# Performance work log

Hardware: AMD Instinct MI355X
Metric: run time of the kernel (lower is better)

## Reference

```python
import jax, jax.numpy as jnp
import numpy as np

B, L, H_IN, H_RED, H_MLP = 2, 1024, 768, 128, 256

def setup_inputs() -> dict:
    key = jax.random.key(0)
    ks = jax.random.split(key, 7)
    s_in = 1.0 / np.sqrt(H_IN)
    s_p = 1.0 / np.sqrt(2 * H_RED)
    s_m = 1.0 / np.sqrt(H_MLP)
    return {
        "inputs": jax.random.normal(ks[0], (B, L, H_IN), dtype=jnp.float32),
        "Wr": jax.random.uniform(ks[1], (H_RED, H_IN), jnp.float32, -s_in, s_in),
        "br": jax.random.uniform(ks[2], (H_RED,), jnp.float32, -s_in, s_in),
        "W1": jax.random.uniform(ks[3], (H_MLP, 2 * H_RED), jnp.float32, -s_p, s_p),
        "b1": jax.random.uniform(ks[4], (H_MLP,), jnp.float32, -s_p, s_p),
        "W2": jax.random.uniform(ks[5], (1, H_MLP), jnp.float32, -s_m, s_m),
        "b2": jax.random.uniform(ks[6], (1,), jnp.float32, -s_m, s_m),
    }

def reference(inputs, Wr, br, W1, b1, W2, b2):
    # pre_reduction: [B,L,H_IN] -> [B,L,H_RED]
    e = jnp.einsum("blh,rh->blr", inputs, Wr) + br
    b_, l_, r_ = e.shape
    # pairwise concat: row i gets e[i], col j gets e[j] -> [B,L,L,2R]
    row = jnp.broadcast_to(e[:, :, None, :], (b_, l_, l_, r_))
    col = jnp.broadcast_to(e[:, None, :, :], (b_, l_, l_, r_))
    pair = jnp.concatenate([row, col], axis=-1)
    # Lin2D: Linear(2R,256) -> ReLU -> Linear(256,1)
    h = jax.nn.relu(jnp.einsum("bijc,mc->bijm", pair, W1) + b1)
    out = jnp.einsum("bijm,om->bijo", h, W2) + b2  # [B,L,L,1]
    out = out[..., 0]  # [B,L,L]
    # symmetrize: triu(out) + triu(out,1)^T
    upper = jnp.triu(out)
    lower = jnp.swapaxes(jnp.triu(out, k=1), -1, -2)
    return upper + lower
```

## Files before the change

kernel.cpp:

```cpp
#include <hip/hip_runtime.h>

typedef __attribute__((ext_vector_type(4))) float f32x4;
typedef __attribute__((ext_vector_type(8))) short bf16x8;

__device__ inline unsigned short f2bf(float x) {
  unsigned u = __builtin_bit_cast(unsigned, x);
  u += 0x7fffu + ((u >> 16) & 1u);
  return (unsigned short)(u >> 16);
}

__device__ inline bf16x8 cvt8(const float* __restrict__ p) {
  f32x4 lo = *(const f32x4*)p;
  f32x4 hi = *(const f32x4*)(p + 4);
  bf16x8 r;
  r[0] = (short)f2bf(lo[0]); r[1] = (short)f2bf(lo[1]);
  r[2] = (short)f2bf(lo[2]); r[3] = (short)f2bf(lo[3]);
  r[4] = (short)f2bf(hi[0]); r[5] = (short)f2bf(hi[1]);
  r[6] = (short)f2bf(hi[2]); r[7] = (short)f2bf(hi[3]);
  return r;
}

__global__ __launch_bounds__(256) void gemm1_kernel(
    const float* __restrict__ X, const float* __restrict__ Wr,
    const float* __restrict__ br, unsigned short* __restrict__ Ebf) {
  int wave = threadIdx.x >> 6;
  int lane = threadIdx.x & 63;
  int t0 = (blockIdx.x * 4 + wave) * 16;
  int n0 = blockIdx.y * 16;
  int lrow = lane & 15;
  int kgrp = (lane >> 4) * 8;
  const float* arow = X + (size_t)(t0 + lrow) * 768 + kgrp;
  const float* brow = Wr + (size_t)(n0 + lrow) * 768 + kgrp;
  f32x4 acc = {0.f, 0.f, 0.f, 0.f};
  for (int k0 = 0; k0 < 768; k0 += 32) {
    bf16x8 a = cvt8(arow + k0);
    bf16x8 b = cvt8(brow + k0);
    acc = __builtin_amdgcn_mfma_f32_16x16x32_bf16(a, b, acc, 0, 0, 0);
  }
  int cn = lane & 15;
  int rbase = (lane >> 4) * 4;
  float bias = br[n0 + cn];
#pragma unroll
  for (int r = 0; r < 4; ++r) {
    float val = acc[r] + bias;
    Ebf[(size_t)(t0 + rbase + r) * 128 + n0 + cn] = f2bf(val);
  }
}

__global__ __launch_bounds__(256) void gemm2_kernel(
    const unsigned short* __restrict__ Ebf, const float* __restrict__ W1,
    const float* __restrict__ b1, float* __restrict__ UVt) {
  int wave = threadIdx.x >> 6;
  int lane = threadIdx.x & 63;
  int t0 = blockIdx.x * 64 + wave * 16;
  int m0 = blockIdx.y * 16;
  int lidx = lane & 15;
  int kg = (lane >> 4) * 8;
  const float* aBase = (m0 < 256)
      ? (W1 + (size_t)(m0 + lidx) * 256 + kg)
      : (W1 + (size_t)(m0 - 256 + lidx) * 256 + 128 + kg);
  const unsigned short* bBase = Ebf + (size_t)(t0 + lidx) * 128 + kg;
  f32x4 acc = {0.f, 0.f, 0.f, 0.f};
  for (int k0 = 0; k0 < 128; k0 += 32) {
    bf16x8 a = cvt8(aBase + k0);
    bf16x8 b = *(const bf16x8*)(const void*)(bBase + k0);
    acc = __builtin_amdgcn_mfma_f32_16x16x32_bf16(a, b, acc, 0, 0, 0);
  }
  int ct = lane & 15;
  int rb = (lane >> 4) * 4;
#pragma unroll
  for (int r = 0; r < 4; ++r) {
    int m = m0 + rb + r;
    float bias = (m < 256) ? b1[m] : 0.f;
    UVt[(size_t)m * 2048 + t0 + ct] = acc[r] + bias;
  }
}

__global__ __launch_bounds__(256) void pairwise_kernel(
    const float* __restrict__ UVt, const float* __restrict__ W2,
    const float* __restrict__ b2p, float* __restrict__ Out) {
  __shared__ float u_lds[64][32];
  __shared__ float v_lds[64][32];
  __shared__ float w2_lds[256];
  __shared__ float t_lds[32][36];

  int tid = threadIdx.x;
  int b = blockIdx.y;
  int p = blockIdx.x;
  int it = 0;
  while (p >= 32 - it) { p -= 32 - it; ++it; }
  int jt = it + p;

  w2_lds[tid] = W2[tid];

  int tx = tid & 15, ty = tid >> 4;
  int q = tid & 7, row = tid >> 3;
  int utok = b * 1024 + it * 32;
  int vtok = b * 1024 + jt * 32;

  float acc00 = 0.f, acc01 = 0.f, acc10 = 0.f, acc11 = 0.f;

  for (int mc = 0; mc < 4; ++mc) {
    __syncthreads();
#pragma unroll
    for (int ph = 0; ph < 2; ++ph) {
      int ml = row + 32 * ph;
      int mg = mc * 64 + ml;
      f32x4 uu = *(const f32x4*)(UVt + (size_t)mg * 2048 + utok + 4 * q);
      f32x4 vv = *(const f32x4*)(UVt + (size_t)(256 + mg) * 2048 + vtok + 4 * q);
      *(f32x4*)&u_lds[ml][4 * q] = uu;
      *(f32x4*)&v_lds[ml][4 * q] = vv;
    }
    __syncthreads();
    for (int mm = 0; mm < 64; mm += 4) {
      f32x4 w2v = *(const f32x4*)&w2_lds[mc * 64 + mm];
#pragma unroll
      for (int t = 0; t < 4; ++t) {
        float u0 = u_lds[mm + t][2 * ty];
        float u1 = u_lds[mm + t][2 * ty + 1];
        float v0 = v_lds[mm + t][2 * tx];
        float v1 = v_lds[mm + t][2 * tx + 1];
        float w = w2v[t];
        acc00 = fmaf(fmaxf(u0 + v0, 0.f), w, acc00);
        acc01 = fmaf(fmaxf(u0 + v1, 0.f), w, acc01);
        acc10 = fmaf(fmaxf(u1 + v0, 0.f), w, acc10);
        acc11 = fmaf(fmaxf(u1 + v1, 0.f), w, acc11);
      }
    }
  }

  float b2v = b2p[0];
  __syncthreads();
  t_lds[2 * ty][2 * tx] = acc00 + b2v;
  t_lds[2 * ty][2 * tx + 1] = acc01 + b2v;
  t_lds[2 * ty + 1][2 * tx] = acc10 + b2v;
  t_lds[2 * ty + 1][2 * tx + 1] = acc11 + b2v;
  __syncthreads();

  int il = tid >> 3;
  int jq = tid & 7;
  size_t obase = (size_t)b << 20;
  if (it != jt) {
    f32x4 dv, mv;
#pragma unroll
    for (int k = 0; k < 4; ++k) dv[k] = t_lds[il][4 * jq + k];
    *(f32x4*)(Out + obase + (size_t)(it * 32 + il) * 1024 + jt * 32 + 4 * jq) = dv;
#pragma unroll
    for (int k = 0; k < 4; ++k) mv[k] = t_lds[4 * jq + k][il];
    *(f32x4*)(Out + obase + (size_t)(jt * 32 + il) * 1024 + it * 32 + 4 * jq) = mv;
  } else {
#pragma unroll
    for (int k = 0; k < 4; ++k) {
      int jl = 4 * jq + k;
      float v = t_lds[il][jl];
      if (jl >= il) Out[obase + (size_t)(it * 32 + il) * 1024 + jt * 32 + jl] = v;
      if (jl > il)  Out[obase + (size_t)(jt * 32 + jl) * 1024 + it * 32 + il] = v;
    }
  }
}

extern "C" void kernel_launch(void* const* d_in, const int* in_sizes, int n_in,
                              void* d_out, int out_size, void* d_ws, size_t ws_size,
                              hipStream_t stream) {
  (void)in_sizes; (void)n_in; (void)out_size; (void)ws_size;
  const float* X  = (const float*)d_in[0];
  const float* Wr = (const float*)d_in[1];
  const float* br = (const float*)d_in[2];
  const float* W1 = (const float*)d_in[3];
  const float* b1 = (const float*)d_in[4];
  const float* W2 = (const float*)d_in[5];
  const float* b2 = (const float*)d_in[6];
  float* Out = (float*)d_out;

  unsigned short* Ebf = (unsigned short*)d_ws;
  float* UVt = (float*)((char*)d_ws + (size_t)2048 * 128 * 2);

  gemm1_kernel<<<dim3(32, 8), 256, 0, stream>>>(X, Wr, br, Ebf);
  gemm2_kernel<<<dim3(32, 32), 256, 0, stream>>>(Ebf, W1, b1, UVt);
  pairwise_kernel<<<dim3(528, 2), 256, 0, stream>>>(UVt, W2, b2, Out);
}
```

Baseline: 57.71 us.

## Use relu=(x+|x|)/2 split, LDS-tiled GEMMs, and smaller pairwise tiles

The pairwise ReLU is rewritten as 0.5*(x+|x|). The linear part is precomputed per token in a new cvec kernel, leaving only one fabs-add-fma per element in the O(L^2) loop. gemm1 now stages bf16 tiles in LDS with register prefetch and computes 64x64 tiles per block, and gemm2 reuses each W1 fragment across four token tiles. The pairwise kernel moves to 16x16 tiles with 64-thread blocks and vectorized LDS reads, which adds an extra launch and changes occupancy and tile overheads.

```diff
diff --git a/kernel.cpp b/kernel.cpp
--- a/kernel.cpp
+++ b/kernel.cpp
@@ -9,9 +9,7 @@
   return (unsigned short)(u >> 16);
 }
 
-__device__ inline bf16x8 cvt8(const float* __restrict__ p) {
-  f32x4 lo = *(const f32x4*)p;
-  f32x4 hi = *(const f32x4*)(p + 4);
+__device__ inline bf16x8 pack8(f32x4 lo, f32x4 hi) {
   bf16x8 r;
   r[0] = (short)f2bf(lo[0]); r[1] = (short)f2bf(lo[1]);
   r[2] = (short)f2bf(lo[2]); r[3] = (short)f2bf(lo[3]);
@@ -20,141 +18,211 @@
   return r;
 }
 
+__device__ inline bf16x8 cvt8(const float* __restrict__ p) {
+  return pack8(*(const f32x4*)p, *(const f32x4*)(p + 4));
+}
+
 __global__ __launch_bounds__(256) void gemm1_kernel(
     const float* __restrict__ X, const float* __restrict__ Wr,
     const float* __restrict__ br, unsigned short* __restrict__ Ebf) {
-  int wave = threadIdx.x >> 6;
-  int lane = threadIdx.x & 63;
-  int t0 = (blockIdx.x * 4 + wave) * 16;
-  int n0 = blockIdx.y * 16;
-  int lrow = lane & 15;
-  int kgrp = (lane >> 4) * 8;
-  const float* arow = X + (size_t)(t0 + lrow) * 768 + kgrp;
-  const float* brow = Wr + (size_t)(n0 + lrow) * 768 + kgrp;
-  f32x4 acc = {0.f, 0.f, 0.f, 0.f};
-  for (int k0 = 0; k0 < 768; k0 += 32) {
-    bf16x8 a = cvt8(arow + k0);
-    bf16x8 b = cvt8(brow + k0);
-    acc = __builtin_amdgcn_mfma_f32_16x16x32_bf16(a, b, acc, 0, 0, 0);
-  }
-  int cn = lane & 15;
-  int rbase = (lane >> 4) * 4;
-  float bias = br[n0 + cn];
-#pragma unroll
-  for (int r = 0; r < 4; ++r) {
-    float val = acc[r] + bias;
-    Ebf[(size_t)(t0 + rbase + r) * 128 + n0 + cn] = f2bf(val);
+  __shared__ unsigned short Xs[64][40];
+  __shared__ unsigned short Ws[64][40];
+
+  int tid = threadIdx.x;
+  int wave = tid >> 6, lane = tid & 63;
+  int tok0 = blockIdx.x * 64;
+  int n0 = blockIdx.y * 64;
+
+  int srow = tid >> 2;
+  int scol = (tid & 3) * 8;
+  const float* xp = X + (size_t)(tok0 + srow) * 768 + scol;
+  const float* wp = Wr + (size_t)(n0 + srow) * 768 + scol;
+
+  int lr = lane & 15;
+  int kg = (lane >> 4) * 8;
+
+  f32x4 acc0 = {0,0,0,0}, acc1 = {0,0,0,0}, acc2 = {0,0,0,0}, acc3 = {0,0,0,0};
+
+  f32x4 x0 = *(const f32x4*)xp;
+  f32x4 x1 = *(const f32x4*)(xp + 4);
+  f32x4 w0 = *(const f32x4*)wp;
+  f32x4 w1 = *(const f32x4*)(wp + 4);
+
+  for (int ks = 0; ks < 24; ++ks) {
+    __syncthreads();
+    *(bf16x8*)&Xs[srow][scol] = pack8(x0, x1);
+    *(bf16x8*)&Ws[srow][scol] = pack8(w0, w1);
+    __syncthreads();
+    if (ks < 23) {
+      int off = (ks + 1) * 32;
+      x0 = *(const f32x4*)(xp + off);
+      x1 = *(const f32x4*)(xp + off + 4);
+      w0 = *(const f32x4*)(wp + off);
+      w1 = *(const f32x4*)(wp + off + 4);
+    }
+    bf16x8 a = *(const bf16x8*)&Xs[wave * 16 + lr][kg];
+    bf16x8 b0 = *(const bf16x8*)&Ws[lr][kg];
+    bf16x8 b1 = *(const bf16x8*)&Ws[16 + lr][kg];
+    bf16x8 b2v = *(const bf16x8*)&Ws[32 + lr][kg];
+    bf16x8 b3 = *(const bf16x8*)&Ws[48 + lr][kg];
+    acc0 = __builtin_amdgcn_mfma_f32_16x16x32_bf16(a, b0, acc0, 0, 0, 0);
+    acc1 = __builtin_amdgcn_mfma_f32_16x16x32_bf16(a, b1, acc1, 0, 0, 0);
+    acc2 = __builtin_amdgcn_mfma_f32_16x16x32_bf16(a, b2v, acc2, 0, 0, 0);
+    acc3 = __builtin_amdgcn_mfma_f32_16x16x32_bf16(a, b3, acc3, 0, 0, 0);
+  }
+
+  int rb = (lane >> 4) * 4;
+  f32x4 accs[4] = {acc0, acc1, acc2, acc3};
+#pragma unroll
+  for (int t = 0; t < 4; ++t) {
+    int n = n0 + t * 16 + lr;
+    float bias = br[n];
+#pragma unroll
+    for (int r = 0; r < 4; ++r) {
+      int tok = tok0 + wave * 16 + rb + r;
+      Ebf[(size_t)tok * 128 + n] = f2bf(accs[t][r] + bias);
+    }
   }
 }
 
 __global__ __launch_bounds__(256) void gemm2_kernel(
     const unsigned short* __restrict__ Ebf, const float* __restrict__ W1,
     const float* __restrict__ b1, float* __restrict__ UVt) {
-  int wave = threadIdx.x >> 6;
-  int lane = threadIdx.x & 63;
-  int t0 = blockIdx.x * 64 + wave * 16;
-  int m0 = blockIdx.y * 16;
-  int lidx = lane & 15;
-  int kg = (lane >> 4) * 8;
+  int wave = threadIdx.x >> 6, lane = threadIdx.x & 63;
+  int t0 = blockIdx.x * 64;
+  int m0 = (blockIdx.y * 4 + wave) * 16;
+  int lr = lane & 15, kg = (lane >> 4) * 8;
   const float* aBase = (m0 < 256)
-      ? (W1 + (size_t)(m0 + lidx) * 256 + kg)
-      : (W1 + (size_t)(m0 - 256 + lidx) * 256 + 128 + kg);
-  const unsigned short* bBase = Ebf + (size_t)(t0 + lidx) * 128 + kg;
-  f32x4 acc = {0.f, 0.f, 0.f, 0.f};
+      ? (W1 + (size_t)(m0 + lr) * 256 + kg)
+      : (W1 + (size_t)(m0 - 256 + lr) * 256 + 128 + kg);
+  f32x4 acc[4] = {{0,0,0,0},{0,0,0,0},{0,0,0,0},{0,0,0,0}};
+#pragma unroll
   for (int k0 = 0; k0 < 128; k0 += 32) {
     bf16x8 a = cvt8(aBase + k0);
-    bf16x8 b = *(const bf16x8*)(const void*)(bBase + k0);
-    acc = __builtin_amdgcn_mfma_f32_16x16x32_bf16(a, b, acc, 0, 0, 0);
-  }
-  int ct = lane & 15;
+#pragma unroll
+    for (int t = 0; t < 4; ++t) {
+      bf16x8 b = *(const bf16x8*)(const void*)(Ebf + (size_t)(t0 + t * 16 + lr) * 128 + kg + k0);
+      acc[t] = __builtin_amdgcn_mfma_f32_16x16x32_bf16(a, b, acc[t], 0, 0, 0);
+    }
+  }
   int rb = (lane >> 4) * 4;
 #pragma unroll
-  for (int r = 0; r < 4; ++r) {
-    int m = m0 + rb + r;
-    float bias = (m < 256) ? b1[m] : 0.f;
-    UVt[(size_t)m * 2048 + t0 + ct] = acc[r] + bias;
-  }
-}
-
-__global__ __launch_bounds__(256) void pairwise_kernel(
+  for (int t = 0; t < 4; ++t) {
+#pragma unroll
+    for (int r = 0; r < 4; ++r) {
+      int m = m0 + rb + r;
+      float bias = (m < 256) ? b1[m] : 0.f;
+      UVt[(size_t)m * 2048 + t0 + t * 16 + lr] = acc[t][r] + bias;
+    }
+  }
+}
+
+__global__ __launch_bounds__(256) void cvec_kernel(
     const float* __restrict__ UVt, const float* __restrict__ W2,
-    const float* __restrict__ b2p, float* __restrict__ Out) {
-  __shared__ float u_lds[64][32];
-  __shared__ float v_lds[64][32];
-  __shared__ float w2_lds[256];
-  __shared__ float t_lds[32][36];
+    const float* __restrict__ b2p, float* __restrict__ cvec) {
+  int h = blockIdx.y;
+  int tok = blockIdx.x * 256 + threadIdx.x;
+  const float* base = UVt + (size_t)h * 256 * 2048 + tok;
+  float a0 = 0.f, a1 = 0.f, a2 = 0.f, a3 = 0.f;
+#pragma unroll 4
+  for (int m = 0; m < 256; m += 4) {
+    a0 = fmaf(W2[m], base[(size_t)m * 2048], a0);
+    a1 = fmaf(W2[m + 1], base[(size_t)(m + 1) * 2048], a1);
+    a2 = fmaf(W2[m + 2], base[(size_t)(m + 2) * 2048], a2);
+    a3 = fmaf(W2[m + 3], base[(size_t)(m + 3) * 2048], a3);
+  }
+  float r = 0.5f * ((a0 + a1) + (a2 + a3)) + (h == 0 ? b2p[0] : 0.f);
+  cvec[h * 2048 + tok] = r;
+}
+
+__global__ __launch_bounds__(64) void pairwise_kernel(
+    const float* __restrict__ UVt, const float* __restrict__ W2,
+    const float* __restrict__ cvec, float* __restrict__ Out) {
+  __shared__ float u_s[16][132];
+  __shared__ float v_s[16][132];
+  __shared__ float w2_s[256];
+  __shared__ float t_s[16][17];
 
   int tid = threadIdx.x;
   int b = blockIdx.y;
   int p = blockIdx.x;
   int it = 0;
-  while (p >= 32 - it) { p -= 32 - it; ++it; }
+  while (p >= 64 - it) { p -= 64 - it; ++it; }
   int jt = it + p;
 
-  w2_lds[tid] = W2[tid];
-
-  int tx = tid & 15, ty = tid >> 4;
-  int q = tid & 7, row = tid >> 3;
-  int utok = b * 1024 + it * 32;
-  int vtok = b * 1024 + jt * 32;
+  *(f32x4*)&w2_s[4 * tid] = *(const f32x4*)&W2[4 * tid];
+
+  int tx = tid & 7, ty = tid >> 3;
+  int utok = b * 1024 + it * 16;
+  int vtok = b * 1024 + jt * 16;
+
+  int mrow = tid >> 2;
+  int tokq = (tid & 3) * 4;
 
   float acc00 = 0.f, acc01 = 0.f, acc10 = 0.f, acc11 = 0.f;
 
-  for (int mc = 0; mc < 4; ++mc) {
-    __syncthreads();
-#pragma unroll
-    for (int ph = 0; ph < 2; ++ph) {
-      int ml = row + 32 * ph;
-      int mg = mc * 64 + ml;
-      f32x4 uu = *(const f32x4*)(UVt + (size_t)mg * 2048 + utok + 4 * q);
-      f32x4 vv = *(const f32x4*)(UVt + (size_t)(256 + mg) * 2048 + vtok + 4 * q);
-      *(f32x4*)&u_lds[ml][4 * q] = uu;
-      *(f32x4*)&v_lds[ml][4 * q] = vv;
-    }
-    __syncthreads();
-    for (int mm = 0; mm < 64; mm += 4) {
-      f32x4 w2v = *(const f32x4*)&w2_lds[mc * 64 + mm];
-#pragma unroll
-      for (int t = 0; t < 4; ++t) {
-        float u0 = u_lds[mm + t][2 * ty];
-        float u1 = u_lds[mm + t][2 * ty + 1];
-        float v0 = v_lds[mm + t][2 * tx];
-        float v1 = v_lds[mm + t][2 * tx + 1];
-        float w = w2v[t];
-        acc00 = fmaf(fmaxf(u0 + v0, 0.f), w, acc00);
-        acc01 = fmaf(fmaxf(u0 + v1, 0.f), w, acc01);
-        acc10 = fmaf(fmaxf(u1 + v0, 0.f), w, acc10);
-        acc11 = fmaf(fmaxf(u1 + v1, 0.f), w, acc11);
+  for (int mc = 0; mc < 2; ++mc) {
+    int M0 = mc * 128;
+    __syncthreads();
+#pragma unroll
+    for (int g = 0; g < 8; ++g) {
+      int ml = g * 16 + mrow;
+      int m = M0 + ml;
+      f32x4 uu = *(const f32x4*)(UVt + (size_t)m * 2048 + utok + tokq);
+      f32x4 vv = *(const f32x4*)(UVt + (size_t)(256 + m) * 2048 + vtok + tokq);
+#pragma unroll
+      for (int k = 0; k < 4; ++k) {
+        u_s[tokq + k][ml] = uu[k];
+        v_s[tokq + k][ml] = vv[k];
       }
     }
-  }
-
-  float b2v = b2p[0];
+    __syncthreads();
+#pragma unroll 8
+    for (int g = 0; g < 32; ++g) {
+      f32x4 wv = *(const f32x4*)&w2_s[M0 + 4 * g];
+      f32x4 ua = *(const f32x4*)&u_s[2 * ty][4 * g];
+      f32x4 ub = *(const f32x4*)&u_s[2 * ty + 1][4 * g];
+      f32x4 va = *(const f32x4*)&v_s[2 * tx][4 * g];
+      f32x4 vb = *(const f32x4*)&v_s[2 * tx + 1][4 * g];
+#pragma unroll
+      for (int k = 0; k < 4; ++k) {
+        acc00 = fmaf(wv[k], fabsf(ua[k] + va[k]), acc00);
+        acc01 = fmaf(wv[k], fabsf(ua[k] + vb[k]), acc01);
+        acc10 = fmaf(wv[k], fabsf(ub[k] + va[k]), acc10);
+        acc11 = fmaf(wv[k], fabsf(ub[k] + vb[k]), acc11);
+      }
+    }
+  }
+
+  float cu0 = cvec[utok + 2 * ty], cu1 = cvec[utok + 2 * ty + 1];
+  float cv0 = cvec[2048 + vtok + 2 * tx], cv1 = cvec[2048 + vtok + 2 * tx + 1];
+
   __syncthreads();
-  t_lds[2 * ty][2 * tx] = acc00 + b2v;
-  t_lds[2 * ty][2 * tx + 1] = acc01 + b2v;
-  t_lds[2 * ty + 1][2 * tx] = acc10 + b2v;
-  t_lds[2 * ty + 1][2 * tx + 1] = acc11 + b2v;
+  t_s[2 * ty][2 * tx]         = cu0 + cv0 + 0.5f * acc00;
+  t_s[2 * ty][2 * tx + 1]     = cu0 + cv1 + 0.5f * acc01;
+  t_s[2 * ty + 1][2 * tx]     = cu1 + cv0 + 0.5f * acc10;
+  t_s[2 * ty + 1][2 * tx + 1] = cu1 + cv1 + 0.5f * acc11;
   __syncthreads();
 
-  int il = tid >> 3;
-  int jq = tid & 7;
+  int il = tid >> 2;
+  int jq = tid & 3;
   size_t obase = (size_t)b << 20;
   if (it != jt) {
     f32x4 dv, mv;
 #pragma unroll
-    for (int k = 0; k < 4; ++k) dv[k] = t_lds[il][4 * jq + k];
-    *(f32x4*)(Out + obase + (size_t)(it * 32 + il) * 1024 + jt * 32 + 4 * jq) = dv;
-#pragma unroll
-    for (int k = 0; k < 4; ++k) mv[k] = t_lds[4 * jq + k][il];
-    *(f32x4*)(Out + obase + (size_t)(jt * 32 + il) * 1024 + it * 32 + 4 * jq) = mv;
+    for (int k = 0; k < 4; ++k) {
+      dv[k] = t_s[il][4 * jq + k];
+      mv[k] = t_s[4 * jq + k][il];
+    }
+    *(f32x4*)(Out + obase + (size_t)(it * 16 + il) * 1024 + jt * 16 + 4 * jq) = dv;
+    *(f32x4*)(Out + obase + (size_t)(jt * 16 + il) * 1024 + it * 16 + 4 * jq) = mv;
   } else {
 #pragma unroll
     for (int k = 0; k < 4; ++k) {
       int jl = 4 * jq + k;
-      float v = t_lds[il][jl];
-      if (jl >= il) Out[obase + (size_t)(it * 32 + il) * 1024 + jt * 32 + jl] = v;
-      if (jl > il)  Out[obase + (size_t)(jt * 32 + jl) * 1024 + it * 32 + il] = v;
+      float v = t_s[il][jl];
+      if (jl >= il) Out[obase + (size_t)(it * 16 + il) * 1024 + it * 16 + jl] = v;
+      if (jl > il)  Out[obase + (size_t)(it * 16 + jl) * 1024 + it * 16 + il] = v;
     }
   }
 }
@@ -174,8 +242,10 @@
 
   unsigned short* Ebf = (unsigned short*)d_ws;
   float* UVt = (float*)((char*)d_ws + (size_t)2048 * 128 * 2);
-
-  gemm1_kernel<<<dim3(32, 8), 256, 0, stream>>>(X, Wr, br, Ebf);
-  gemm2_kernel<<<dim3(32, 32), 256, 0, stream>>>(Ebf, W1, b1, UVt);
-  pairwise_kernel<<<dim3(528, 2), 256, 0, stream>>>(UVt, W2, b2, Out);
-}
+  float* cvec = (float*)((char*)d_ws + (size_t)2048 * 128 * 2 + (size_t)512 * 2048 * 4);
+
+  gemm1_kernel<<<dim3(32, 2), 256, 0, stream>>>(X, Wr, br, Ebf);
+  gemm2_kernel<<<dim3(32, 8), 256, 0, stream>>>(Ebf, W1, b1, UVt);
+  cvec_kernel<<<dim3(8, 2), 256, 0, stream>>>(UVt, W2, b2, cvec);
+  pairwise_kernel<<<dim3(2080, 2), 64, 0, stream>>>(UVt, W2, cvec, Out);
+}
```

Result: slower. 71.57 us (+24.0%).

## Rewrite ReLU as abs identity, hoist linear terms, and retile all kernels

Applied to the files above, without the earlier changes.

The pairwise ReLU is rewritten with relu(x) = 0.5(x+|x|). The linear parts (0.5·W2·u and 0.5·W2·v) are reduced inside gemm2 into a per-token vector with atomics, so the pairwise inner loop only accumulates w·|u+v|, and abs can be a free operand modifier. A separate prep kernel converts X, Wr and W1 to bf16 once. The GEMMs are retiled so each wave computes four MFMA tiles. The pairwise kernel splits the hidden dimension across waves with 4x4 register tiles, then reduces through LDS. In exchange it adds an extra kernel launch plus a memset, and relies on float atomics whose summation order is nondeterministic.

```diff
diff --git a/kernel.cpp b/kernel.cpp
--- a/kernel.cpp
+++ b/kernel.cpp
@@ -9,9 +9,7 @@
   return (unsigned short)(u >> 16);
 }
 
-__device__ inline bf16x8 cvt8(const float* __restrict__ p) {
-  f32x4 lo = *(const f32x4*)p;
-  f32x4 hi = *(const f32x4*)(p + 4);
+__device__ inline bf16x8 pack8(f32x4 lo, f32x4 hi) {
   bf16x8 r;
   r[0] = (short)f2bf(lo[0]); r[1] = (short)f2bf(lo[1]);
   r[2] = (short)f2bf(lo[2]); r[3] = (short)f2bf(lo[3]);
@@ -20,141 +18,222 @@
   return r;
 }
 
+__global__ __launch_bounds__(256) void prep_kernel(
+    const float* __restrict__ X, const float* __restrict__ Wr,
+    const float* __restrict__ W1, const float* __restrict__ W2,
+    unsigned short* __restrict__ Xbf, unsigned short* __restrict__ Wrbf,
+    unsigned short* __restrict__ W1bf, float* __restrict__ w2h) {
+  int bid = blockIdx.x, tid = threadIdx.x;
+  if (bid < 768) {
+    size_t o = (size_t)bid * 2048 + tid * 8;
+    f32x4 a = *(const f32x4*)(X + o), b = *(const f32x4*)(X + o + 4);
+    *(bf16x8*)(Xbf + o) = pack8(a, b);
+  } else if (bid < 816) {
+    size_t o = (size_t)(bid - 768) * 2048 + tid * 8;
+    f32x4 a = *(const f32x4*)(Wr + o), b = *(const f32x4*)(Wr + o + 4);
+    *(bf16x8*)(Wrbf + o) = pack8(a, b);
+  } else if (bid < 848) {
+    size_t o = (size_t)(bid - 816) * 2048 + tid * 8;
+    int m = (int)(o >> 7), k = (int)(o & 127);
+    const float* src = (m < 256) ? (W1 + (size_t)m * 256 + k)
+                                 : (W1 + (size_t)(m - 256) * 256 + 128 + k);
+    f32x4 a = *(const f32x4*)src, b = *(const f32x4*)(src + 4);
+    *(bf16x8*)(W1bf + o) = pack8(a, b);
+  } else {
+    w2h[tid] = 0.5f * W2[tid];
+  }
+}
+
 __global__ __launch_bounds__(256) void gemm1_kernel(
-    const float* __restrict__ X, const float* __restrict__ Wr,
+    const unsigned short* __restrict__ Xbf, const unsigned short* __restrict__ Wrbf,
     const float* __restrict__ br, unsigned short* __restrict__ Ebf) {
-  int wave = threadIdx.x >> 6;
-  int lane = threadIdx.x & 63;
-  int t0 = (blockIdx.x * 4 + wave) * 16;
-  int n0 = blockIdx.y * 16;
-  int lrow = lane & 15;
-  int kgrp = (lane >> 4) * 8;
-  const float* arow = X + (size_t)(t0 + lrow) * 768 + kgrp;
-  const float* brow = Wr + (size_t)(n0 + lrow) * 768 + kgrp;
-  f32x4 acc = {0.f, 0.f, 0.f, 0.f};
+  int wave = threadIdx.x >> 6, lane = threadIdx.x & 63;
+  int tok0 = (blockIdx.x * 4 + wave) * 16;
+  int n0 = blockIdx.y * 64;
+  int lr = lane & 15, kg = (lane >> 4) * 8;
+  const unsigned short* ap = Xbf + (size_t)(tok0 + lr) * 768 + kg;
+  const unsigned short* bp0 = Wrbf + (size_t)(n0 + lr) * 768 + kg;
+  const unsigned short* bp1 = bp0 + 16 * 768;
+  const unsigned short* bp2 = bp0 + 32 * 768;
+  const unsigned short* bp3 = bp0 + 48 * 768;
+  f32x4 acc0 = {0,0,0,0}, acc1 = {0,0,0,0}, acc2 = {0,0,0,0}, acc3 = {0,0,0,0};
+#pragma unroll 4
   for (int k0 = 0; k0 < 768; k0 += 32) {
-    bf16x8 a = cvt8(arow + k0);
-    bf16x8 b = cvt8(brow + k0);
-    acc = __builtin_amdgcn_mfma_f32_16x16x32_bf16(a, b, acc, 0, 0, 0);
-  }
-  int cn = lane & 15;
-  int rbase = (lane >> 4) * 4;
-  float bias = br[n0 + cn];
-#pragma unroll
-  for (int r = 0; r < 4; ++r) {
-    float val = acc[r] + bias;
-    Ebf[(size_t)(t0 + rbase + r) * 128 + n0 + cn] = f2bf(val);
+    bf16x8 a = *(const bf16x8*)(ap + k0);
+    bf16x8 b0 = *(const bf16x8*)(bp0 + k0);
+    bf16x8 b1 = *(const bf16x8*)(bp1 + k0);
+    bf16x8 b2 = *(const bf16x8*)(bp2 + k0);
+    bf16x8 b3 = *(const bf16x8*)(bp3 + k0);
+    acc0 = __builtin_amdgcn_mfma_f32_16x16x32_bf16(a, b0, acc0, 0, 0, 0);
+    acc1 = __builtin_amdgcn_mfma_f32_16x16x32_bf16(a, b1, acc1, 0, 0, 0);
+    acc2 = __builtin_amdgcn_mfma_f32_16x16x32_bf16(a, b2, acc2, 0, 0, 0);
+    acc3 = __builtin_amdgcn_mfma_f32_16x16x32_bf16(a, b3, acc3, 0, 0, 0);
+  }
+  int rb = (lane >> 4) * 4;
+  f32x4 accs[4] = {acc0, acc1, acc2, acc3};
+#pragma unroll
+  for (int t = 0; t < 4; ++t) {
+    int n = n0 + t * 16 + lr;
+    float bias = br[n];
+#pragma unroll
+    for (int r = 0; r < 4; ++r)
+      Ebf[(size_t)(tok0 + rb + r) * 128 + n] = f2bf(accs[t][r] + bias);
   }
 }
 
 __global__ __launch_bounds__(256) void gemm2_kernel(
-    const unsigned short* __restrict__ Ebf, const float* __restrict__ W1,
-    const float* __restrict__ b1, float* __restrict__ UVt) {
-  int wave = threadIdx.x >> 6;
-  int lane = threadIdx.x & 63;
-  int t0 = blockIdx.x * 64 + wave * 16;
-  int m0 = blockIdx.y * 16;
-  int lidx = lane & 15;
-  int kg = (lane >> 4) * 8;
-  const float* aBase = (m0 < 256)
-      ? (W1 + (size_t)(m0 + lidx) * 256 + kg)
-      : (W1 + (size_t)(m0 - 256 + lidx) * 256 + 128 + kg);
-  const unsigned short* bBase = Ebf + (size_t)(t0 + lidx) * 128 + kg;
-  f32x4 acc = {0.f, 0.f, 0.f, 0.f};
+    const unsigned short* __restrict__ Ebf, const unsigned short* __restrict__ W1bf,
+    const float* __restrict__ b1, const float* __restrict__ w2h,
+    float* __restrict__ UVt, float* __restrict__ cvec) {
+  int wave = threadIdx.x >> 6, lane = threadIdx.x & 63;
+  int t0 = blockIdx.x * 64;
+  int m0 = (blockIdx.y * 4 + wave) * 16;
+  int lr = lane & 15, kg = (lane >> 4) * 8;
+  const unsigned short* aB = W1bf + (size_t)(m0 + lr) * 128 + kg;
+  f32x4 acc[4] = {{0,0,0,0},{0,0,0,0},{0,0,0,0},{0,0,0,0}};
+#pragma unroll
   for (int k0 = 0; k0 < 128; k0 += 32) {
-    bf16x8 a = cvt8(aBase + k0);
-    bf16x8 b = *(const bf16x8*)(const void*)(bBase + k0);
-    acc = __builtin_amdgcn_mfma_f32_16x16x32_bf16(a, b, acc, 0, 0, 0);
-  }
-  int ct = lane & 15;
+    bf16x8 a = *(const bf16x8*)(aB + k0);
+#pragma unroll
+    for (int t = 0; t < 4; ++t) {
+      bf16x8 b = *(const bf16x8*)(Ebf + (size_t)(t0 + t * 16 + lr) * 128 + kg + k0);
+      acc[t] = __builtin_amdgcn_mfma_f32_16x16x32_bf16(a, b, acc[t], 0, 0, 0);
+    }
+  }
   int rb = (lane >> 4) * 4;
-#pragma unroll
-  for (int r = 0; r < 4; ++r) {
-    int m = m0 + rb + r;
-    float bias = (m < 256) ? b1[m] : 0.f;
-    UVt[(size_t)m * 2048 + t0 + ct] = acc[r] + bias;
+  float p[4] = {0.f, 0.f, 0.f, 0.f};
+#pragma unroll
+  for (int t = 0; t < 4; ++t) {
+#pragma unroll
+    for (int r = 0; r < 4; ++r) {
+      int m = m0 + rb + r;
+      float val = acc[t][r] + ((m0 < 256) ? b1[m] : 0.f);
+      UVt[(size_t)m * 2048 + t0 + t * 16 + lr] = val;
+      p[t] = fmaf(w2h[m & 255], val, p[t]);
+    }
+  }
+#pragma unroll
+  for (int t = 0; t < 4; ++t) {
+    p[t] += __shfl_xor(p[t], 16);
+    p[t] += __shfl_xor(p[t], 32);
+  }
+  if (lane < 16) {
+    int h = (m0 < 256) ? 0 : 1;
+#pragma unroll
+    for (int t = 0; t < 4; ++t)
+      atomicAdd(&cvec[h * 2048 + t0 + t * 16 + lane], p[t]);
   }
 }
 
 __global__ __launch_bounds__(256) void pairwise_kernel(
-    const float* __restrict__ UVt, const float* __restrict__ W2,
-    const float* __restrict__ b2p, float* __restrict__ Out) {
-  __shared__ float u_lds[64][32];
-  __shared__ float v_lds[64][32];
-  __shared__ float w2_lds[256];
-  __shared__ float t_lds[32][36];
+    const float* __restrict__ UVt, const float* __restrict__ w2h,
+    const float* __restrict__ cvec, const float* __restrict__ b2p,
+    float* __restrict__ Out) {
+  __shared__ float u_s[4][64][36];
+  __shared__ float v_s[4][64][36];
+  __shared__ float w2_s[256];
+  __shared__ float cuv[64];
 
   int tid = threadIdx.x;
+  int wave = tid >> 6, lane = tid & 63;
   int b = blockIdx.y;
   int p = blockIdx.x;
   int it = 0;
   while (p >= 32 - it) { p -= 32 - it; ++it; }
   int jt = it + p;
 
-  w2_lds[tid] = W2[tid];
-
-  int tx = tid & 15, ty = tid >> 4;
-  int q = tid & 7, row = tid >> 3;
   int utok = b * 1024 + it * 32;
   int vtok = b * 1024 + jt * 32;
 
-  float acc00 = 0.f, acc01 = 0.f, acc10 = 0.f, acc11 = 0.f;
-
-  for (int mc = 0; mc < 4; ++mc) {
-    __syncthreads();
-#pragma unroll
-    for (int ph = 0; ph < 2; ++ph) {
-      int ml = row + 32 * ph;
-      int mg = mc * 64 + ml;
-      f32x4 uu = *(const f32x4*)(UVt + (size_t)mg * 2048 + utok + 4 * q);
-      f32x4 vv = *(const f32x4*)(UVt + (size_t)(256 + mg) * 2048 + vtok + 4 * q);
-      *(f32x4*)&u_lds[ml][4 * q] = uu;
-      *(f32x4*)&v_lds[ml][4 * q] = vv;
-    }
-    __syncthreads();
-    for (int mm = 0; mm < 64; mm += 4) {
-      f32x4 w2v = *(const f32x4*)&w2_lds[mc * 64 + mm];
-#pragma unroll
-      for (int t = 0; t < 4; ++t) {
-        float u0 = u_lds[mm + t][2 * ty];
-        float u1 = u_lds[mm + t][2 * ty + 1];
-        float v0 = v_lds[mm + t][2 * tx];
-        float v1 = v_lds[mm + t][2 * tx + 1];
-        float w = w2v[t];
-        acc00 = fmaf(fmaxf(u0 + v0, 0.f), w, acc00);
-        acc01 = fmaf(fmaxf(u0 + v1, 0.f), w, acc01);
-        acc10 = fmaf(fmaxf(u1 + v0, 0.f), w, acc10);
-        acc11 = fmaf(fmaxf(u1 + v1, 0.f), w, acc11);
+  w2_s[tid] = w2h[tid];
+  if (tid < 32) cuv[tid] = cvec[utok + tid];
+  else if (tid < 64) cuv[tid] = cvec[2048 + vtok + (tid - 32)];
+
+  int mr = lane >> 3, tq = (lane & 7) * 4;
+#pragma unroll
+  for (int g = 0; g < 8; ++g) {
+    int ml = g * 8 + mr;
+    int m = wave * 64 + ml;
+    *(f32x4*)&u_s[wave][ml][tq] = *(const f32x4*)(UVt + (size_t)m * 2048 + utok + tq);
+    *(f32x4*)&v_s[wave][ml][tq] = *(const f32x4*)(UVt + (size_t)(256 + m) * 2048 + vtok + tq);
+  }
+  __syncthreads();
+
+  int tx = lane & 7, ty = lane >> 3;
+  float acc[4][4] = {{0,0,0,0},{0,0,0,0},{0,0,0,0},{0,0,0,0}};
+  for (int ml = 0; ml < 64; ml += 4) {
+    f32x4 wq = *(const f32x4*)&w2_s[wave * 64 + ml];
+#pragma unroll
+    for (int s = 0; s < 4; ++s) {
+      f32x4 uu = *(const f32x4*)&u_s[wave][ml + s][4 * ty];
+      f32x4 vv = *(const f32x4*)&v_s[wave][ml + s][4 * tx];
+      float w = wq[s];
+#pragma unroll
+      for (int i = 0; i < 4; ++i)
+#pragma unroll
+        for (int j = 0; j < 4; ++j)
+          acc[i][j] = fmaf(w, fabsf(uu[i] + vv[j]), acc[i][j]);
+    }
+  }
+
+  __syncthreads();
+  float* ov = (float*)u_s;
+  if (wave > 0) {
+#pragma unroll
+    for (int i = 0; i < 4; ++i) {
+      f32x4 rowv = {acc[i][0], acc[i][1], acc[i][2], acc[i][3]};
+      *(f32x4*)&ov[(((wave - 1) * 4 + i) * 64 + lane) * 4] = rowv;
+    }
+  }
+  __syncthreads();
+  if (wave == 0) {
+#pragma unroll
+    for (int w = 1; w < 4; ++w)
+#pragma unroll
+      for (int i = 0; i < 4; ++i) {
+        f32x4 rowv = *(const f32x4*)&ov[(((w - 1) * 4 + i) * 64 + lane) * 4];
+#pragma unroll
+        for (int j = 0; j < 4; ++j) acc[i][j] += rowv[j];
       }
-    }
-  }
-
-  float b2v = b2p[0];
-  __syncthreads();
-  t_lds[2 * ty][2 * tx] = acc00 + b2v;
-  t_lds[2 * ty][2 * tx + 1] = acc01 + b2v;
-  t_lds[2 * ty + 1][2 * tx] = acc10 + b2v;
-  t_lds[2 * ty + 1][2 * tx + 1] = acc11 + b2v;
-  __syncthreads();
-
-  int il = tid >> 3;
-  int jq = tid & 7;
-  size_t obase = (size_t)b << 20;
-  if (it != jt) {
-    f32x4 dv, mv;
-#pragma unroll
-    for (int k = 0; k < 4; ++k) dv[k] = t_lds[il][4 * jq + k];
-    *(f32x4*)(Out + obase + (size_t)(it * 32 + il) * 1024 + jt * 32 + 4 * jq) = dv;
-#pragma unroll
-    for (int k = 0; k < 4; ++k) mv[k] = t_lds[4 * jq + k][il];
-    *(f32x4*)(Out + obase + (size_t)(jt * 32 + il) * 1024 + it * 32 + 4 * jq) = mv;
-  } else {
-#pragma unroll
-    for (int k = 0; k < 4; ++k) {
-      int jl = 4 * jq + k;
-      float v = t_lds[il][jl];
-      if (jl >= il) Out[obase + (size_t)(it * 32 + il) * 1024 + jt * 32 + jl] = v;
-      if (jl > il)  Out[obase + (size_t)(jt * 32 + jl) * 1024 + it * 32 + il] = v;
+    float b2v = b2p[0];
+    float val[4][4];
+#pragma unroll
+    for (int i = 0; i < 4; ++i)
+#pragma unroll
+      for (int j = 0; j < 4; ++j)
+        val[i][j] = acc[i][j] + cuv[4 * ty + i] + cuv[32 + 4 * tx + j] + b2v;
+
+    size_t obase = (size_t)b << 20;
+    int i0 = it * 32, j0 = jt * 32;
+    if (it != jt) {
+#pragma unroll
+      for (int i = 0; i < 4; ++i) {
+        f32x4 dv = {val[i][0], val[i][1], val[i][2], val[i][3]};
+        *(f32x4*)(Out + obase + (size_t)(i0 + 4 * ty + i) * 1024 + j0 + 4 * tx) = dv;
+      }
+      float* t32 = (float*)v_s;
+#pragma unroll
+      for (int i = 0; i < 4; ++i)
+#pragma unroll
+        for (int j = 0; j < 4; ++j)
+          t32[(4 * ty + i) * 33 + 4 * tx + j] = val[i][j];
+      __builtin_amdgcn_s_waitcnt(0);
+#pragma unroll
+      for (int i = 0; i < 4; ++i) {
+        f32x4 mv;
+#pragma unroll
+        for (int k = 0; k < 4; ++k) mv[k] = t32[(4 * tx + k) * 33 + 4 * ty + i];
+        *(f32x4*)(Out + obase + (size_t)(j0 + 4 * ty + i) * 1024 + i0 + 4 * tx) = mv;
+      }
+    } else {
+#pragma unroll
+      for (int i = 0; i < 4; ++i)
+#pragma unroll
+        for (int j = 0; j < 4; ++j) {
+          int il = 4 * ty + i, jl = 4 * tx + j;
+          if (jl >= il) Out[obase + (size_t)(i0 + il) * 1024 + j0 + jl] = val[i][j];
+          if (jl > il)  Out[obase + (size_t)(j0 + jl) * 1024 + i0 + il] = val[i][j];
+        }
     }
   }
 }
@@ -172,10 +251,18 @@
   const float* b2 = (const float*)d_in[6];
   float* Out = (float*)d_out;
 
-  unsigned short* Ebf = (unsigned short*)d_ws;
-  float* UVt = (float*)((char*)d_ws + (size_t)2048 * 128 * 2);
-
-  gemm1_kernel<<<dim3(32, 8), 256, 0, stream>>>(X, Wr, br, Ebf);
-  gemm2_kernel<<<dim3(32, 32), 256, 0, stream>>>(Ebf, W1, b1, UVt);
-  pairwise_kernel<<<dim3(528, 2), 256, 0, stream>>>(UVt, W2, b2, Out);
-}
+  char* ws = (char*)d_ws;
+  unsigned short* Xbf  = (unsigned short*)(ws);
+  unsigned short* Wrbf = (unsigned short*)(ws + 3145728);
+  unsigned short* W1bf = (unsigned short*)(ws + 3342336);
+  float*          w2h  = (float*)(ws + 3473408);
+  unsigned short* Ebf  = (unsigned short*)(ws + 3474432);
+  float*          UVt  = (float*)(ws + 3998720);
+  float*          cvec = (float*)(ws + 8193024);
+
+  prep_kernel<<<849, 256, 0, stream>>>(X, Wr, W1, W2, Xbf, Wrbf, W1bf, w2h);
+  hipMemsetAsync(cvec, 0, 2 * 2048 * sizeof(float), stream);
+  gemm1_kernel<<<dim3(32, 2), 256, 0, stream>>>(Xbf, Wrbf, br, Ebf);
+  gemm2_kernel<<<dim3(32, 8), 256, 0, stream>>>(Ebf, W1bf, b1, w2h, UVt, cvec);
+  pairwise_kernel<<<dim3(528, 2), 256, 0, stream>>>(UVt, w2h, cvec, b2, Out);
+}
```

After: 64.99 us. 12.6% more time.
